# Kernel tuning notes

Measured on AMD Instinct MI355X. Metric: run time of the kernel, lower is better.

The kernel has to match this reference:

```python
import jax, jax.numpy as jnp
import numpy as np
from jax import lax

WIN = 7  # hard-coded winsize in PSF.forward
EPS = 1e-8


def _box_sum(x, n):
    # Sliding n x n window sum with zero padding (== ZeroPad2d(n//2) + unfold sum),
    return lax.reduce_window(x, 0.0, lax.add, (1, 1, n, n), (1, 1, 1, 1), 'SAME')


def _patch_stats(x, n):
    n2 = n * n
    s = _box_sum(x, n)
    s2 = _box_sum(x * x, n)
    mean = s / n2
    # torch .var() default is unbiased (divide by N-1)
    var = (s2 - n2 * mean * mean) / (n2 - 1)
    return mean, jnp.maximum(var, 0.0)


def patch_mv_norm(x, n):
    mean, var = _patch_stats(x, n)
    return (x - mean) / (jnp.sqrt(var) + EPS)


def patch_adain(x, y, n):
    x_norm = patch_mv_norm(x, n)
    y_mean, y_var = _patch_stats(y, n)
    return x_norm * jnp.sqrt(y_var) + y_mean  # note: no eps on y_std, as in source


def conv1x1(x, w, b):
    # x: (B,C,H,W), w: (O,C), b: (O,)
    return jnp.einsum('oc,bchw->bohw', w, x) + b[None, :, None, None]


def setup_inputs() -> dict:
    key = jax.random.key(0)
    ks = jax.random.split(key, 12)
    B, C, H, W = 8, 256, 128, 128
    front = jax.random.normal(ks[0], (B, C, H, W), dtype=jnp.float32)
    back = jax.random.normal(ks[1], (B, C, H, W), dtype=jnp.float32)
    mask = jax.random.uniform(ks[2], (B, 1, H, W), dtype=jnp.float32)
    scale = 0.02
    we = jax.random.normal(ks[3], (C, C), dtype=jnp.float32) * scale
    wf = jax.random.normal(ks[4], (C, C), dtype=jnp.float32) * scale
    wg = jax.random.normal(ks[5], (C, C), dtype=jnp.float32) * scale
    wh = jax.random.normal(ks[6], (C, C), dtype=jnp.float32) * scale
    be = jax.random.normal(ks[7], (C,), dtype=jnp.float32) * scale
    bf = jax.random.normal(ks[8], (C,), dtype=jnp.float32) * scale
    bg = jax.random.normal(ks[9], (C,), dtype=jnp.float32) * scale
    bh = jax.random.normal(ks[10], (C,), dtype=jnp.float32) * scale
    return {'front': front, 'back': back, 'mask': mask,
            'we': we, 'be': be, 'wf': wf, 'bf': bf,
            'wg': wg, 'bg': bg, 'wh': wh, 'bh': bh}


def reference(front, back, mask, we, be, wf, bf, wg, bg, wh, bh):
    b, c, h, w = front.shape
    EE = conv1x1(patch_adain(front, back, WIN), we, be)
    FF = conv1x1(patch_mv_norm(front, WIN), wf, bf)
    GG = conv1x1(patch_mv_norm(back, WIN), wg, bg)
    HH = conv1x1(back, wh, bh)
    # channel-wise cosine similarity between FF and GG
    F_n = jnp.sqrt(jnp.sum(FF * FF, axis=1))  # (B,H,W)
    G_n = jnp.sqrt(jnp.sum(GG * GG, axis=1))
    S = jnp.sum(FF * GG, axis=1) / (F_n * G_n)
    # per-sample spatial min-max normalization
    S_flat = S.reshape(b, h * w)
    s_min = jnp.min(S_flat, axis=1, keepdims=True)
    s_max = jnp.max(S_flat, axis=1, keepdims=True)
    S_n = ((S_flat - s_min) / (s_max - s_min)).reshape(b, 1, h, w)
    fused = S_n * EE + (1.0 - S_n) * HH
    return fused
```

## Files before the change

### kernel.cpp

```cpp
#include <hip/hip_runtime.h>
#include <math.h>

#define PIX 16384
#define TSZ ((size_t)33554432)

typedef __attribute__((ext_vector_type(8))) short  short8;
typedef __attribute__((ext_vector_type(4))) float  float4v;
typedef __attribute__((ext_vector_type(4))) unsigned int uint4v;
typedef __attribute__((ext_vector_type(2))) unsigned int uint2v;

__device__ __forceinline__ unsigned short f2bf(float x) {
  unsigned int u = __float_as_uint(x);
  u += 0x7fffu + ((u >> 16) & 1u);
  return (unsigned short)(u >> 16);
}
__device__ __forceinline__ float bf2f(unsigned short h) {
  return __uint_as_float(((unsigned int)h) << 16);
}
__device__ __forceinline__ unsigned int pack_bf2(float lo, float hi) {
  unsigned int ul = __float_as_uint(lo); ul += 0x7fffu + ((ul >> 16) & 1u);
  unsigned int uh = __float_as_uint(hi); uh += 0x7fffu + ((uh >> 16) & 1u);
  return __builtin_amdgcn_perm(uh, ul, 0x07060302u);
}

#define SB0   __builtin_amdgcn_sched_barrier(0)
#define BARR  __builtin_amdgcn_s_barrier()
#define LGKM0 asm volatile("s_waitcnt lgkmcnt(0)" ::: "memory")
#define VMC(n) asm volatile("s_waitcnt vmcnt(" #n ")" ::: "memory")

__global__ __launch_bounds__(256) void k_prep(const float* __restrict__ we,
                                              const float* __restrict__ wf,
                                              const float* __restrict__ wg,
                                              const float* __restrict__ wh,
                                              unsigned short* __restrict__ wbf) {
  int idx = blockIdx.x * 256 + threadIdx.x;
  int g = idx >> 16, within = idx & 65535;
  const float* src = (g == 0) ? wf : (g == 1) ? wg : (g == 2) ? we : wh;
  int e    = within & 7;
  int lane = (within >> 3) & 63;
  int im   = (within >> 9) & 3;
  int wv   = (within >> 11) & 3;
  int i    = within >> 13;
  int col = lane & 15, q = lane >> 4;
  int m = wv * 64 + im * 16 + col;
  int k = i * 32 + q * 8 + e;
  wbf[idx] = f2bf(src[m * 256 + k]);
}

__global__ __launch_bounds__(256, 4) void k_stats(const float* __restrict__ front,
                                                  const float* __restrict__ back,
                                                  unsigned short* __restrict__ xcm) {
  int blk = blockIdx.x;
  int s   = blk & 7;
  int c   = (blk >> 3) & 255;
  int b   = blk >> 11;
  int t   = threadIdx.x;
  int r0  = s * 16;

  __shared__ float2 vspD[16 * 137];

  size_t planeOff = ((size_t)(b * 256 + c)) * PIX;

  float meanR[8], sdR[8];

  #pragma unroll 1
  for (int phase = 0; phase < 2; ++phase) {
    const float* src = (phase == 0 ? back : front) + planeOff;
    {
      int col = t & 127;
      int rg  = (t >> 7) * 8;
      const float* colp = src + col;
      float xv[14];
      #pragma unroll
      for (int j = 0; j < 14; ++j) {
        int g = r0 + rg - 3 + j;
        float v = 0.f;
        if (g >= 0 && g < 128) v = colp[g * 128];
        xv[j] = v;
      }
      float sm = 0.f, s2 = 0.f;
      #pragma unroll
      for (int j = 0; j < 7; ++j) { sm += xv[j]; s2 = fmaf(xv[j], xv[j], s2); }
      vspD[rg * 137 + col + 3] = make_float2(sm, s2);
      #pragma unroll
      for (int o = 1; o < 8; ++o) {
        float vn = xv[o + 6], vo = xv[o - 1];
        sm += vn - vo;
        s2 += vn * vn - vo * vo;
        vspD[(rg + o) * 137 + col + 3] = make_float2(sm, s2);
      }
      if (t < 96) {
        int rr = t & 15;
        int pc = t >> 4;
        int ac = (pc < 3) ? pc : 128 + pc;
        vspD[rr * 137 + ac] = make_float2(0.f, 0.f);
      }
    }
    LGKM0; BARR;
    {
      int r  = t & 15;
      int c0 = (t >> 4) * 8;
      float2 w[14];
      #pragma unroll
      for (int i = 0; i < 14; ++i) w[i] = vspD[r * 137 + c0 + i];
      float4v x0 = *(const float4v*)(src + (r0 + r) * 128 + c0);
      float4v x1 = *(const float4v*)(src + (r0 + r) * 128 + c0 + 4);
      float xc[8] = {x0[0], x0[1], x0[2], x0[3], x1[0], x1[1], x1[2], x1[3]};
      float sm = 0.f, s2 = 0.f;
      #pragma unroll
      for (int i = 0; i < 7; ++i) { sm += w[i].x; s2 += w[i].y; }
      float nrmv[8], hv[8];
      #pragma unroll
      for (int o = 0; o < 8; ++o) {
        float mean = sm * (1.f / 49.f);
        float var  = (s2 - sm * mean) * (1.f / 48.f);
        var = var > 0.f ? var : 0.f;
        float sd = __builtin_amdgcn_sqrtf(var);
        float x  = xc[o];
        float nrm = (x - mean) * __builtin_amdgcn_rcpf(sd + 1e-8f);
        if (phase == 0) { meanR[o] = mean; sdR[o] = sd; hv[o] = x; }
        else            { hv[o] = nrm * sdR[o] + meanR[o]; }
        nrmv[o] = nrm;
        if (o < 7) { sm += w[o + 7].x - w[o].x; s2 += w[o + 7].y - w[o].y; }
      }
      uint4v nv  = (uint4v){pack_bf2(nrmv[0], nrmv[1]), pack_bf2(nrmv[2], nrmv[3]),
                            pack_bf2(nrmv[4], nrmv[5]), pack_bf2(nrmv[6], nrmv[7])};
      uint4v hvv = (uint4v){pack_bf2(hv[0], hv[1]), pack_bf2(hv[2], hv[3]),
                            pack_bf2(hv[4], hv[5]), pack_bf2(hv[6], hv[7])};
      int p = (r0 + r) * 128 + c0;
      size_t gb2 = (((size_t)(b * 256 + (p >> 6))) * 256 + c) * 64 + (p & 63);
      int tn0 = (phase == 0) ? 1 : 0;
      int tn1 = (phase == 0) ? 3 : 2;
      *(uint4v*)(xcm + (size_t)tn0 * TSZ + gb2) = nv;
      *(uint4v*)(xcm + (size_t)tn1 * TSZ + gb2) = hvv;
    }
    LGKM0; BARR;
  }
}

__device__ __forceinline__ void stage_tile(const unsigned short* __restrict__ Xt,
                                           int k0, int t,
                                           unsigned short* dst) {
  int kk = ((t >> 5) << 2) + ((t & 7) >> 1);
  int px = (((t >> 3) & 3) << 4) + ((t & 1) << 3);
  const unsigned short* src = Xt + (size_t)(k0 << 6) + (kk << 6) + px;
  typedef const __attribute__((address_space(1))) unsigned int GUI;
  typedef __attribute__((address_space(3))) unsigned int LUI;
  __builtin_amdgcn_global_load_lds((GUI*)(unsigned long long)src,
                                   (LUI*)(unsigned)(unsigned long long)(dst + t * 8),
                                   16, 0, 0);
}

#define LOADA(S, I) {                                           \
  af[S][0] = *(const short8*)(Wr + (I) * 8192 + 0 * 512);       \
  af[S][1] = *(const short8*)(Wr + (I) * 8192 + 1 * 512);       \
  af[S][2] = *(const short8*)(Wr + (I) * 8192 + 2 * 512);       \
  af[S][3] = *(const short8*)(Wr + (I) * 8192 + 3 * 512); }

#define TR8(O0,O1,O2,O3,O4,O5,O6,O7)                                              \
  asm volatile("ds_read_b64_tr_b16 %0, %1 offset:" #O0 : "=v"(r0) : "v"(tra));    \
  asm volatile("ds_read_b64_tr_b16 %0, %1 offset:" #O1 : "=v"(r1) : "v"(tra));    \
  asm volatile("ds_read_b64_tr_b16 %0, %1 offset:" #O2 : "=v"(r2) : "v"(tra));    \
  asm volatile("ds_read_b64_tr_b16 %0, %1 offset:" #O3 : "=v"(r3) : "v"(tra));    \
  asm volatile("ds_read_b64_tr_b16 %0, %1 offset:" #O4 : "=v"(r4) : "v"(tra));    \
  asm volatile("ds_read_b64_tr_b16 %0, %1 offset:" #O5 : "=v"(r5) : "v"(tra));    \
  asm volatile("ds_read_b64_tr_b16 %0, %1 offset:" #O6 : "=v"(r6) : "v"(tra));    \
  asm volatile("ds_read_b64_tr_b16 %0, %1 offset:" #O7 : "=v"(r7) : "v"(tra));

#define DOMFMA(MS) {                                                        \
  union BU { unsigned u[4]; short8 s; } bu0, bu1, bu2, bu3;                 \
  bu0.u[0]=r0[0]; bu0.u[1]=r0[1]; bu0.u[2]=r1[0]; bu0.u[3]=r1[1];           \
  bu1.u[0]=r2[0]; bu1.u[1]=r2[1]; bu1.u[2]=r3[0]; bu1.u[3]=r3[1];           \
  bu2.u[0]=r4[0]; bu2.u[1]=r4[1]; bu2.u[2]=r5[0]; bu2.u[3]=r5[1];           \
  bu3.u[0]=r6[0]; bu3.u[1]=r6[1]; bu3.u[2]=r7[0]; bu3.u[3]=r7[1];           \
  short8 bv0 = bu0.s, bv1 = bu1.s, bv2 = bu2.s, bv3 = bu3.s;                \
  _Pragma("unroll")                                                         \
  for (int im = 0; im < 4; ++im) {                                          \
    acc[0][im] = __builtin_amdgcn_mfma_f32_16x16x32_bf16(af[MS][im], bv0, acc[0][im], 0, 0, 0); \
    acc[1][im] = __builtin_amdgcn_mfma_f32_16x16x32_bf16(af[MS][im], bv1, acc[1][im], 0, 0, 0); \
    acc[2][im] = __builtin_amdgcn_mfma_f32_16x16x32_bf16(af[MS][im], bv2, acc[2][im], 0, 0, 0); \
    acc[3][im] = __builtin_amdgcn_mfma_f32_16x16x32_bf16(af[MS][im], bv3, acc[3][im], 0, 0, 0); \
  } }

__device__ __forceinline__ void gemm_pipe(const unsigned short* __restrict__ X,
                                          const unsigned short* __restrict__ Wm,
                                          unsigned short* xt, unsigned xbase,
                                          int mbase, int lane, int t,
                                          float4v acc[4][4]) {
  unsigned tra = xbase + (unsigned)((((lane >> 4)) << 10) + ((lane & 15) << 3));
  const unsigned short* __restrict__ Wr = Wm + ((mbase >> 6) << 11) + lane * 8;

  short8 af[2][4];
  uint2v r0, r1, r2, r3, r4, r5, r6, r7;

  #pragma unroll
  for (int in = 0; in < 4; ++in)
    #pragma unroll
    for (int im = 0; im < 4; ++im)
      acc[in][im] = (float4v){0.f, 0.f, 0.f, 0.f};

  SB0; BARR; SB0;
  stage_tile(X,   0, t, xt + 0 * 2048);
  stage_tile(X,  32, t, xt + 1 * 2048);
  stage_tile(X,  64, t, xt + 2 * 2048);
  stage_tile(X,  96, t, xt + 3 * 2048);
  SB0;

  LOADA(0, 0); LOADA(1, 1);
  SB0;
  stage_tile(X, 128, t, xt + 4 * 2048);
  stage_tile(X, 160, t, xt + 5 * 2048);
  SB0;
  VMC(2); SB0; BARR; SB0;
  TR8(    0,   512,   128,   640,   256,   768,   384,   896); LGKM0; SB0; DOMFMA(0);
  TR8( 4096,  4608,  4224,  4736,  4352,  4864,  4480,  4992); LGKM0; SB0; DOMFMA(1);

  SB0;
  LOADA(0, 2); LOADA(1, 3);
  SB0;
  stage_tile(X, 192, t, xt + 6 * 2048);
  stage_tile(X, 224, t, xt + 7 * 2048);
  SB0;
  VMC(2); SB0; BARR; SB0;
  TR8( 8192,  8704,  8320,  8832,  8448,  8960,  8576,  9088); LGKM0; SB0; DOMFMA(0);
  TR8(12288, 12800, 12416, 12928, 12544, 13056, 12672, 13184); LGKM0; SB0; DOMFMA(1);

  SB0;
  LOADA(0, 4); LOADA(1, 5);
  SB0;
  VMC(0); SB0; BARR; SB0;
  TR8(16384, 16896, 16512, 17024, 16640, 17152, 16768, 17280); LGKM0; SB0; DOMFMA(0);
  TR8(20480, 20992, 20608, 21120, 20736, 21248, 20864, 21376); LGKM0; SB0; DOMFMA(1);

  SB0;
  LOADA(0, 6); LOADA(1, 7);
  SB0;
  VMC(0); SB0; BARR; SB0;
  TR8(24576, 25088, 24704, 25216, 24832, 25344, 24960, 25472); LGKM0; SB0; DOMFMA(0);
  TR8(28672, 29184, 28800, 29312, 28928, 29440, 29056, 29568); LGKM0; SB0; DOMFMA(1);
}

__global__ __launch_bounds__(256, 2) void k_gemm1(const unsigned short* __restrict__ xcm,
                                                  const unsigned short* __restrict__ wbf,
                                                  const float* __restrict__ bFF,
                                                  const float* __restrict__ bGG,
                                                  float* __restrict__ Sout) {
  int blk  = blockIdx.x;
  int b    = blk >> 8;
  int pt   = blk & 255;
  int p0   = pt * 64;
  int t    = threadIdx.x;
  int wv   = t >> 6;
  int lane = t & 63;
  int q    = lane >> 4;
  int mbase = wv * 64;

  __shared__ __align__(16) unsigned short xt[8][2048];
  __shared__ float sred[3 * 64];
  if (t < 192) sred[t] = 0.f;
  __syncthreads();
  unsigned xbase = (unsigned)(unsigned long long)&xt[0][0];

  const unsigned short* Xt = xcm + (((size_t)(b * 256 + pt)) << 14);

  float4v aF[4][4], aG[4][4];

  gemm_pipe(Xt + 0 * TSZ, wbf + 0 * 65536, &xt[0][0], xbase, mbase, lane, t, aF);
  gemm_pipe(Xt + 1 * TSZ, wbf + 1 * 65536, &xt[0][0], xbase, mbase, lane, t, aG);
  #pragma unroll
  for (int im = 0; im < 4; ++im) {
    float4v bvF = *(const float4v*)(bFF + mbase + im * 16 + q * 4);
    float4v bvG = *(const float4v*)(bGG + mbase + im * 16 + q * 4);
    #pragma unroll
    for (int in = 0; in < 4; ++in) { aF[in][im] += bvF; aG[in][im] += bvG; }
  }
  #pragma unroll
  for (int in = 0; in < 4; ++in) {
    float d = 0.f, nf = 0.f, ng = 0.f;
    #pragma unroll
    for (int im = 0; im < 4; ++im)
      #pragma unroll
      for (int r = 0; r < 4; ++r) {
        float f = aF[in][im][r], g = aG[in][im][r];
        d += f * g; nf += f * f; ng += g * g;
      }
    d  += __shfl_xor(d, 16);  d  += __shfl_xor(d, 32);
    nf += __shfl_xor(nf, 16); nf += __shfl_xor(nf, 32);
    ng += __shfl_xor(ng, 16); ng += __shfl_xor(ng, 32);
    if (lane < 16) {
      atomicAdd(&sred[0 * 64 + in * 16 + lane], d);
      atomicAdd(&sred[1 * 64 + in * 16 + lane], nf);
      atomicAdd(&sred[2 * 64 + in * 16 + lane], ng);
    }
  }
  __syncthreads();
  if (t < 64) {
    float d = sred[t], nf = sred[64 + t], ng = sred[128 + t];
    Sout[(size_t)b * PIX + p0 + t] = d / (sqrtf(nf) * sqrtf(ng));
  }
}

__global__ __launch_bounds__(256, 2) void k_gemm2(const unsigned short* __restrict__ xcm,
                                                  const unsigned short* __restrict__ wbf,
                                                  const float* __restrict__ bEE,
                                                  const float* __restrict__ bHH,
                                                  const float* __restrict__ S,
                                                  const float* __restrict__ mm,
                                                  float* __restrict__ out) {
  int blk  = blockIdx.x;
  int b    = blk >> 8;
  int pt   = blk & 255;
  int p0   = pt * 64;
  int t    = threadIdx.x;
  int wv   = t >> 6;
  int lane = t & 63;
  int col  = lane & 15;
  int q    = lane >> 4;
  int mbase = wv * 64;

  __shared__ __align__(16) unsigned short xt[8][2048];
  unsigned xbase = (unsigned)(unsigned long long)&xt[0][0];

  const unsigned short* Xt = xcm + (((size_t)(b * 256 + pt)) << 14);

  float4v aE[4][4], aH[4][4];

  gemm_pipe(Xt + 2 * TSZ, wbf + 2 * 65536, &xt[0][0], xbase, mbase, lane, t, aE);
  gemm_pipe(Xt + 3 * TSZ, wbf + 3 * 65536, &xt[0][0], xbase, mbase, lane, t, aH);

  float mn = mm[b * 2], mx = mm[b * 2 + 1];
  float inv = 1.f / (mx - mn);
  float sn[4];
  #pragma unroll
  for (int in = 0; in < 4; ++in)
    sn[in] = (S[(size_t)b * PIX + p0 + in * 16 + col] - mn) * inv;

  #pragma unroll
  for (int im = 0; im < 4; ++im) {
    float4v bvE = *(const float4v*)(bEE + mbase + im * 16 + q * 4);
    float4v bvH = *(const float4v*)(bHH + mbase + im * 16 + q * 4);
    #pragma unroll
    for (int in = 0; in < 4; ++in)
      #pragma unroll
      for (int r = 0; r < 4; ++r) {
        int m = mbase + im * 16 + q * 4 + r;
        float e = aE[in][im][r] + bvE[r];
        float h = aH[in][im][r] + bvH[r];
        out[((size_t)(b * 256 + m)) * PIX + p0 + in * 16 + col] = h + sn[in] * (e - h);
      }
  }
}

__global__ __launch_bounds__(256) void k_minmax(const float* __restrict__ S,
                                                float* __restrict__ mm) {
  int b = blockIdx.x, t = threadIdx.x;
  const float* sp = S + (size_t)b * PIX;
  float mn = 3.0e38f, mx = -3.0e38f;
  for (int i = t; i < PIX; i += 256) { float v = sp[i]; mn = fminf(mn, v); mx = fmaxf(mx, v); }
  #pragma unroll
  for (int o = 32; o >= 1; o >>= 1) {
    mn = fminf(mn, __shfl_xor(mn, o));
    mx = fmaxf(mx, __shfl_xor(mx, o));
  }
  __shared__ float smn[4], smx[4];
  if ((t & 63) == 0) { smn[t >> 6] = mn; smx[t >> 6] = mx; }
  __syncthreads();
  if (t == 0) {
    mn = fminf(fminf(smn[0], smn[1]), fminf(smn[2], smn[3]));
    mx = fmaxf(fmaxf(smx[0], smx[1]), fmaxf(smx[2], smx[3]));
    mm[b * 2] = mn; mm[b * 2 + 1] = mx;
  }
}

extern "C" void kernel_launch(void* const* d_in, const int* in_sizes, int n_in,
                              void* d_out, int out_size, void* d_ws, size_t ws_size,
                              hipStream_t stream) {
  const float* front = (const float*)d_in[0];
  const float* back  = (const float*)d_in[1];
  const float* we = (const float*)d_in[3];
  const float* be = (const float*)d_in[4];
  const float* wf = (const float*)d_in[5];
  const float* bf = (const float*)d_in[6];
  const float* wg = (const float*)d_in[7];
  const float* bg = (const float*)d_in[8];
  const float* wh = (const float*)d_in[9];
  const float* bh = (const float*)d_in[10];

  char* ws = (char*)d_ws;
  unsigned short* xcm  = (unsigned short*)(ws);
  unsigned short* wbf  = (unsigned short*)(ws + 268435456);
  float*          S    = (float*)(ws + 268959744);
  float*          mm   = (float*)(ws + 269484032);
  float*          out  = (float*)d_out;

  k_prep  <<<1024,  256, 0, stream>>>(we, wf, wg, wh, wbf);
  k_stats <<<16384, 256, 0, stream>>>(front, back, xcm);
  k_gemm1 <<<2048,  256, 0, stream>>>(xcm, wbf, bf, bg, S);
  k_minmax<<<8,     256, 0, stream>>>(S, mm);
  k_gemm2 <<<2048,  256, 0, stream>>>(xcm, wbf, be, bh, S, mm, out);
}
```

Before: 511.5 us.

## Fold weight prep into stats kernel, fuse min-max via atomics, overlap LDS reads with MFMA

The weight bf16 conversion is merged into the stats kernel as extra blocks, which also initialize the min/max slots. The separate min-max kernel is removed: each gemm1 block reduces its S values and updates per-sample min/max with atomics on order-preserving integer keys. The GEMM inner loop now waits for transposed LDS reads in pairs with partial lgkmcnt counts, so MFMAs can start before all eight reads land. Together these remove two launches and expose more load/compute overlap, at the cost of atomic contention and a tighter instruction schedule.

Result: no change. 504.0 us (median of 2 runs) (-1.5%).

```diff
diff --git a/kernel.cpp b/kernel.cpp
--- a/kernel.cpp
+++ b/kernel.cpp
@@ -23,38 +23,54 @@
   return __builtin_amdgcn_perm(uh, ul, 0x07060302u);
 }
 
+__device__ __forceinline__ unsigned int fkey(float f) {
+  unsigned int u = __float_as_uint(f);
+  return (u & 0x80000000u) ? ~u : (u | 0x80000000u);
+}
+__device__ __forceinline__ float funkey(unsigned int k) {
+  unsigned int u = (k & 0x80000000u) ? (k ^ 0x80000000u) : ~k;
+  return __uint_as_float(u);
+}
+
 #define SB0   __builtin_amdgcn_sched_barrier(0)
 #define BARR  __builtin_amdgcn_s_barrier()
 #define LGKM0 asm volatile("s_waitcnt lgkmcnt(0)" ::: "memory")
+#define LGK(n) asm volatile("s_waitcnt lgkmcnt(" #n ")" ::: "memory")
 #define VMC(n) asm volatile("s_waitcnt vmcnt(" #n ")" ::: "memory")
-
-__global__ __launch_bounds__(256) void k_prep(const float* __restrict__ we,
-                                              const float* __restrict__ wf,
-                                              const float* __restrict__ wg,
-                                              const float* __restrict__ wh,
-                                              unsigned short* __restrict__ wbf) {
-  int idx = blockIdx.x * 256 + threadIdx.x;
-  int g = idx >> 16, within = idx & 65535;
-  const float* src = (g == 0) ? wf : (g == 1) ? wg : (g == 2) ? we : wh;
-  int e    = within & 7;
-  int lane = (within >> 3) & 63;
-  int im   = (within >> 9) & 3;
-  int wv   = (within >> 11) & 3;
-  int i    = within >> 13;
-  int col = lane & 15, q = lane >> 4;
-  int m = wv * 64 + im * 16 + col;
-  int k = i * 32 + q * 8 + e;
-  wbf[idx] = f2bf(src[m * 256 + k]);
-}
 
 __global__ __launch_bounds__(256, 4) void k_stats(const float* __restrict__ front,
                                                   const float* __restrict__ back,
-                                                  unsigned short* __restrict__ xcm) {
+                                                  const float* __restrict__ we,
+                                                  const float* __restrict__ wf,
+                                                  const float* __restrict__ wg,
+                                                  const float* __restrict__ wh,
+                                                  unsigned short* __restrict__ xcm,
+                                                  unsigned short* __restrict__ wbf,
+                                                  unsigned int* __restrict__ mmu) {
   int blk = blockIdx.x;
+  int t   = threadIdx.x;
+
+  if (blk >= 16384) {
+    if (blk == 16384 && t < 16)
+      mmu[t] = (t & 1) ? 0u : 0xFFFFFFFFu;
+    int idx = (blk - 16384) * 256 + t;
+    int g = idx >> 16, within = idx & 65535;
+    const float* src = (g == 0) ? wf : (g == 1) ? wg : (g == 2) ? we : wh;
+    int e    = within & 7;
+    int lane = (within >> 3) & 63;
+    int im   = (within >> 9) & 3;
+    int wv   = (within >> 11) & 3;
+    int i    = within >> 13;
+    int col = lane & 15, q = lane >> 4;
+    int m = wv * 64 + im * 16 + col;
+    int k = i * 32 + q * 8 + e;
+    wbf[idx] = f2bf(src[m * 256 + k]);
+    return;
+  }
+
   int s   = blk & 7;
   int c   = (blk >> 3) & 255;
   int b   = blk >> 11;
-  int t   = threadIdx.x;
   int r0  = s * 16;
 
   __shared__ float2 vspD[16 * 137];
@@ -167,20 +183,21 @@
   asm volatile("ds_read_b64_tr_b16 %0, %1 offset:" #O6 : "=v"(r6) : "v"(tra));    \
   asm volatile("ds_read_b64_tr_b16 %0, %1 offset:" #O7 : "=v"(r7) : "v"(tra));
 
-#define DOMFMA(MS) {                                                        \
-  union BU { unsigned u[4]; short8 s; } bu0, bu1, bu2, bu3;                 \
-  bu0.u[0]=r0[0]; bu0.u[1]=r0[1]; bu0.u[2]=r1[0]; bu0.u[3]=r1[1];           \
-  bu1.u[0]=r2[0]; bu1.u[1]=r2[1]; bu1.u[2]=r3[0]; bu1.u[3]=r3[1];           \
-  bu2.u[0]=r4[0]; bu2.u[1]=r4[1]; bu2.u[2]=r5[0]; bu2.u[3]=r5[1];           \
-  bu3.u[0]=r6[0]; bu3.u[1]=r6[1]; bu3.u[2]=r7[0]; bu3.u[3]=r7[1];           \
-  short8 bv0 = bu0.s, bv1 = bu1.s, bv2 = bu2.s, bv3 = bu3.s;                \
+#define QUAD(MS, IN, RA, RB) {                                              \
+  union BU { unsigned u[4]; short8 s; } bu;                                 \
+  bu.u[0] = RA[0]; bu.u[1] = RA[1]; bu.u[2] = RB[0]; bu.u[3] = RB[1];       \
+  short8 bv = bu.s;                                                         \
   _Pragma("unroll")                                                         \
-  for (int im = 0; im < 4; ++im) {                                          \
-    acc[0][im] = __builtin_amdgcn_mfma_f32_16x16x32_bf16(af[MS][im], bv0, acc[0][im], 0, 0, 0); \
-    acc[1][im] = __builtin_amdgcn_mfma_f32_16x16x32_bf16(af[MS][im], bv1, acc[1][im], 0, 0, 0); \
-    acc[2][im] = __builtin_amdgcn_mfma_f32_16x16x32_bf16(af[MS][im], bv2, acc[2][im], 0, 0, 0); \
-    acc[3][im] = __builtin_amdgcn_mfma_f32_16x16x32_bf16(af[MS][im], bv3, acc[3][im], 0, 0, 0); \
-  } }
+  for (int im = 0; im < 4; ++im)                                            \
+    acc[IN][im] = __builtin_amdgcn_mfma_f32_16x16x32_bf16(af[MS][im], bv, acc[IN][im], 0, 0, 0); \
+}
+
+#define TRMFMA(MS, O0,O1,O2,O3,O4,O5,O6,O7)                                 \
+  TR8(O0,O1,O2,O3,O4,O5,O6,O7);                                             \
+  LGK(6); SB0; QUAD(MS, 0, r0, r1);                                         \
+  LGK(4); SB0; QUAD(MS, 1, r2, r3);                                         \
+  LGK(2); SB0; QUAD(MS, 2, r4, r5);                                         \
+  LGK(0); SB0; QUAD(MS, 3, r6, r7);
 
 __device__ __forceinline__ void gemm_pipe(const unsigned short* __restrict__ X,
                                           const unsigned short* __restrict__ Wm,
@@ -212,8 +229,8 @@
   stage_tile(X, 160, t, xt + 5 * 2048);
   SB0;
   VMC(2); SB0; BARR; SB0;
-  TR8(    0,   512,   128,   640,   256,   768,   384,   896); LGKM0; SB0; DOMFMA(0);
-  TR8( 4096,  4608,  4224,  4736,  4352,  4864,  4480,  4992); LGKM0; SB0; DOMFMA(1);
+  TRMFMA(0,     0,   512,   128,   640,   256,   768,   384,   896)
+  TRMFMA(1,  4096,  4608,  4224,  4736,  4352,  4864,  4480,  4992)
 
   SB0;
   LOADA(0, 2); LOADA(1, 3);
@@ -222,29 +239,30 @@
   stage_tile(X, 224, t, xt + 7 * 2048);
   SB0;
   VMC(2); SB0; BARR; SB0;
-  TR8( 8192,  8704,  8320,  8832,  8448,  8960,  8576,  9088); LGKM0; SB0; DOMFMA(0);
-  TR8(12288, 12800, 12416, 12928, 12544, 13056, 12672, 13184); LGKM0; SB0; DOMFMA(1);
+  TRMFMA(0,  8192,  8704,  8320,  8832,  8448,  8960,  8576,  9088)
+  TRMFMA(1, 12288, 12800, 12416, 12928, 12544, 13056, 12672, 13184)
 
   SB0;
   LOADA(0, 4); LOADA(1, 5);
   SB0;
   VMC(0); SB0; BARR; SB0;
-  TR8(16384, 16896, 16512, 17024, 16640, 17152, 16768, 17280); LGKM0; SB0; DOMFMA(0);
-  TR8(20480, 20992, 20608, 21120, 20736, 21248, 20864, 21376); LGKM0; SB0; DOMFMA(1);
+  TRMFMA(0, 16384, 16896, 16512, 17024, 16640, 17152, 16768, 17280)
+  TRMFMA(1, 20480, 20992, 20608, 21120, 20736, 21248, 20864, 21376)
 
   SB0;
   LOADA(0, 6); LOADA(1, 7);
   SB0;
   VMC(0); SB0; BARR; SB0;
-  TR8(24576, 25088, 24704, 25216, 24832, 25344, 24960, 25472); LGKM0; SB0; DOMFMA(0);
-  TR8(28672, 29184, 28800, 29312, 28928, 29440, 29056, 29568); LGKM0; SB0; DOMFMA(1);
+  TRMFMA(0, 24576, 25088, 24704, 25216, 24832, 25344, 24960, 25472)
+  TRMFMA(1, 28672, 29184, 28800, 29312, 28928, 29440, 29056, 29568)
 }
 
 __global__ __launch_bounds__(256, 2) void k_gemm1(const unsigned short* __restrict__ xcm,
                                                   const unsigned short* __restrict__ wbf,
                                                   const float* __restrict__ bFF,
                                                   const float* __restrict__ bGG,
-                                                  float* __restrict__ Sout) {
+                                                  float* __restrict__ Sout,
+                                                  unsigned int* __restrict__ mmu) {
   int blk  = blockIdx.x;
   int b    = blk >> 8;
   int pt   = blk & 255;
@@ -296,7 +314,18 @@
   __syncthreads();
   if (t < 64) {
     float d = sred[t], nf = sred[64 + t], ng = sred[128 + t];
-    Sout[(size_t)b * PIX + p0 + t] = d / (sqrtf(nf) * sqrtf(ng));
+    float sv = d / (sqrtf(nf) * sqrtf(ng));
+    Sout[(size_t)b * PIX + p0 + t] = sv;
+    float mn = sv, mx = sv;
+    #pragma unroll
+    for (int o = 32; o >= 1; o >>= 1) {
+      mn = fminf(mn, __shfl_xor(mn, o));
+      mx = fmaxf(mx, __shfl_xor(mx, o));
+    }
+    if (t == 0) {
+      atomicMin(&mmu[b * 2],     fkey(mn));
+      atomicMax(&mmu[b * 2 + 1], fkey(mx));
+    }
   }
 }
 
@@ -305,7 +334,7 @@
                                                   const float* __restrict__ bEE,
                                                   const float* __restrict__ bHH,
                                                   const float* __restrict__ S,
-                                                  const float* __restrict__ mm,
+                                                  const unsigned int* __restrict__ mmu,
                                                   float* __restrict__ out) {
   int blk  = blockIdx.x;
   int b    = blk >> 8;
@@ -328,7 +357,7 @@
   gemm_pipe(Xt + 2 * TSZ, wbf + 2 * 65536, &xt[0][0], xbase, mbase, lane, t, aE);
   gemm_pipe(Xt + 3 * TSZ, wbf + 3 * 65536, &xt[0][0], xbase, mbase, lane, t, aH);
 
-  float mn = mm[b * 2], mx = mm[b * 2 + 1];
+  float mn = funkey(mmu[b * 2]), mx = funkey(mmu[b * 2 + 1]);
   float inv = 1.f / (mx - mn);
   float sn[4];
   #pragma unroll
@@ -348,27 +377,6 @@
         float h = aH[in][im][r] + bvH[r];
         out[((size_t)(b * 256 + m)) * PIX + p0 + in * 16 + col] = h + sn[in] * (e - h);
       }
-  }
-}
-
-__global__ __launch_bounds__(256) void k_minmax(const float* __restrict__ S,
-                                                float* __restrict__ mm) {
-  int b = blockIdx.x, t = threadIdx.x;
-  const float* sp = S + (size_t)b * PIX;
-  float mn = 3.0e38f, mx = -3.0e38f;
-  for (int i = t; i < PIX; i += 256) { float v = sp[i]; mn = fminf(mn, v); mx = fmaxf(mx, v); }
-  #pragma unroll
-  for (int o = 32; o >= 1; o >>= 1) {
-    mn = fminf(mn, __shfl_xor(mn, o));
-    mx = fmaxf(mx, __shfl_xor(mx, o));
-  }
-  __shared__ float smn[4], smx[4];
-  if ((t & 63) == 0) { smn[t >> 6] = mn; smx[t >> 6] = mx; }
-  __syncthreads();
-  if (t == 0) {
-    mn = fminf(fminf(smn[0], smn[1]), fminf(smn[2], smn[3]));
-    mx = fmaxf(fmaxf(smx[0], smx[1]), fmaxf(smx[2], smx[3]));
-    mm[b * 2] = mn; mm[b * 2 + 1] = mx;
   }
 }
 
@@ -390,12 +398,10 @@
   unsigned short* xcm  = (unsigned short*)(ws);
   unsigned short* wbf  = (unsigned short*)(ws + 268435456);
   float*          S    = (float*)(ws + 268959744);
-  float*          mm   = (float*)(ws + 269484032);
+  unsigned int*   mmu  = (unsigned int*)(ws + 269484032);
   float*          out  = (float*)d_out;
 
-  k_prep  <<<1024,  256, 0, stream>>>(we, wf, wg, wh, wbf);
-  k_stats <<<16384, 256, 0, stream>>>(front, back, xcm);
-  k_gemm1 <<<2048,  256, 0, stream>>>(xcm, wbf, bf, bg, S);
-  k_minmax<<<8,     256, 0, stream>>>(S, mm);
-  k_gemm2 <<<2048,  256, 0, stream>>>(xcm, wbf, be, bh, S, mm, out);
-}
+  k_stats <<<17408, 256, 0, stream>>>(front, back, we, wf, wg, wh, xcm, wbf, mmu);
+  k_gemm1 <<<2048,  256, 0, stream>>>(xcm, wbf, bf, bg, S, mmu);
+  k_gemm2 <<<2048,  256, 0, stream>>>(xcm, wbf, be, bh, S, mmu, out);
+}
```
